# Kernel optimization log

Hardware: AMD Instinct MI355X
Metric: run time of the kernel (lower is better)

The kernel has to match this reference:

```python
import jax, jax.numpy as jnp
import numpy as np

B, R, NB, T = 32, 96, 5, 2048
FEAT_DIM = 64
SPARSITY = 0.2


def _per_band(X, community, W1, b1, W2, b2):
    # X: [R, T] wavelet coeffs for one (batch, band) slice
    n, t = X.shape
    f32 = X.dtype
    # --- functional connectivity (cosine of centered signals == Pearson corr) ---
    Xc = X - X.mean(axis=1, keepdims=True)
    norm = jnp.linalg.norm(Xc, axis=1, keepdims=True)
    norm = jnp.where(norm == 0, 1.0, norm)
    C = (Xc @ Xc.T) / (norm * norm.T)
    C = jnp.nan_to_num(C, nan=0.0)
    C = C * (1.0 - jnp.eye(n, dtype=f32))  # zero diagonal
    # --- quantile sparsification over strict lower triangle ---
    ti, tj = np.tril_indices(n, -1)
    thr = jnp.quantile(jnp.abs(C[ti, tj]), 1.0 - SPARSITY)
    A = C * (jnp.abs(C) >= thr).astype(f32)  # graph_type == 'weighted'
    # --- node features (5-dim, averaged over regions) ---
    mean_f = X.mean(axis=1)
    std_f = jnp.std(X, axis=1, ddof=1)  # torch.std is unbiased
    energy_f = (X ** 2).sum(axis=1)
    maxamp_f = jnp.abs(X).max(axis=1)
    ps = jnp.abs(jnp.fft.fft(X, axis=1)) ** 2
    ps = ps[:, : t // 2]
    s = ps.sum(axis=1, keepdims=True)
    s = jnp.where(s == 0, 1.0, s)
    p = ps / s
    ent_f = -(p * jnp.log(p + 1e-10)).sum(axis=1)
    node5 = jnp.stack([mean_f, std_f, energy_f, maxamp_f, ent_f], axis=1).mean(axis=0)
    # --- graph properties (6-dim) on binarized adjacency ---
    Bm = (A != 0).astype(f32)
    ne = Bm.sum() / 2.0
    density = ne / (n * (n - 1) / 2.0)
    deg = Bm.sum(axis=1)
    avg_deg = deg.mean()
    A2 = Bm @ Bm
    tri = (A2 * Bm).sum() / 6.0
    poss = (deg * (deg - 1.0)).sum() / 2.0
    clus = jnp.where(poss > 0, tri / jnp.where(poss > 0, poss, 1.0), 0.0)
    # global efficiency: safe reciprocal (zero where A+I == 0; original would emit inf)
    denom = Bm + jnp.eye(n, dtype=f32)
    eff = jnp.where(denom > 0, 1.0 / jnp.where(denom > 0, denom, 1.0), 0.0).sum() / (n * (n - 1))
    # approximate modularity with fixed 2-community assignment (deterministic)
    m2 = 2.0 * ne
    m2_safe = jnp.where(m2 > 0, m2, 1.0)
    same = (community[:, None] == community[None, :]) & (~jnp.eye(n, dtype=bool))
    expected = jnp.outer(deg, deg) / m2_safe
    mod = jnp.where(m2 > 0, (same * (Bm - expected)).sum() / m2_safe, 0.0)
    props = jnp.stack([ne, density, avg_deg, clus, eff, mod])
    feat11 = jnp.concatenate([node5, props])  # [11]
    # --- feature encoder MLP (dropout is identity at inference) ---
    h = jnp.maximum(feat11 @ W1.T + b1, 0.0)
    return A, h @ W2.T + b2


def _forward(wavelet_coeffs, frequency_bands, community, W1, b1, W2, b2):
    b, r, nb, t = wavelet_coeffs.shape
    Xs = wavelet_coeffs.transpose(0, 2, 1, 3).reshape(b * nb, r, t)  # [B*NB, R, T]
    A, F = jax.vmap(_per_band, in_axes=(0, None, None, None, None, None))(
        Xs, community, W1, b1, W2, b2)
    return A.reshape(b, nb, r, r), F.reshape(b, nb, -1)


def setup_inputs() -> dict:
    key = jax.random.key(0)
    k0, k1, k2, k3, k4 = jax.random.split(key, 5)
    wavelet_coeffs = jax.random.normal(k0, (B, R, NB, T), dtype=jnp.float32)
    frequency_bands = jax.random.uniform(k1, (NB, 2), dtype=jnp.float32)
    community = jax.random.randint(k2, (R,), 0, 2)
    W1 = jax.random.normal(k3, (32, 11), dtype=jnp.float32) * 0.3
    b1 = jnp.zeros((32,), jnp.float32)
    W2 = jax.random.normal(k4, (FEAT_DIM, 32), dtype=jnp.float32) * 0.18
    b2 = jnp.zeros((FEAT_DIM,), jnp.float32)
    return {"wavelet_coeffs": wavelet_coeffs, "frequency_bands": frequency_bands,
            "community": community, "W1": W1, "b1": b1, "W2": W2, "b2": b2}


def reference(wavelet_coeffs, frequency_bands, community, W1, b1, W2, b2):
    return _forward(wavelet_coeffs, frequency_bands, community, W1, b1, W2, b2)
```

## Files before the change

### kernel.cpp

```cpp
#include <hip/hip_runtime.h>
#include <hip/hip_bf16.h>
#include <math.h>
#include <float.h>

#ifndef M_PI
#define M_PI 3.14159265358979323846
#endif

#define NBANDS 160
#define RR 96
#define TT 2048
#define NTRIL 4560
#define A_ELEMS ((size_t)NBANDS * RR * RR)
#define NBIN 8192
#define MAXCAND 512
#define BKS 64
#define NST (TT / BKS)
#define GPITCH 76
#define FBLK 256

#define PHI(L) ((L) ^ (((L) >> 5) & 31))

typedef float  f32x4  __attribute__((ext_vector_type(4)));
typedef __bf16 bf16x8 __attribute__((ext_vector_type(8)));
typedef __bf16 bf16x4 __attribute__((ext_vector_type(4)));

__device__ inline void blockReduceSum4(double v0, double v1, double v2, double v3,
                                       double* sred, double out[4]) {
    for (int off = 32; off > 0; off >>= 1) {
        v0 += __shfl_down(v0, off, 64);
        v1 += __shfl_down(v1, off, 64);
        v2 += __shfl_down(v2, off, 64);
        v3 += __shfl_down(v3, off, 64);
    }
    int lane = threadIdx.x & 63, wid = threadIdx.x >> 6;
    int nw = blockDim.x >> 6;
    if (lane == 0) {
        sred[wid * 4 + 0] = v0; sred[wid * 4 + 1] = v1;
        sred[wid * 4 + 2] = v2; sred[wid * 4 + 3] = v3;
    }
    __syncthreads();
    if (threadIdx.x < 4) {
        double r = sred[threadIdx.x];
        for (int w = 1; w < nw; w++) r += sred[w * 4 + threadIdx.x];
        sred[nw * 4 + threadIdx.x] = r;
    }
    __syncthreads();
    out[0] = sred[nw * 4 + 0]; out[1] = sred[nw * 4 + 1];
    out[2] = sred[nw * 4 + 2]; out[3] = sred[nw * 4 + 3];
    __syncthreads();
}

__device__ inline void blockReduceSum2(double v0, double v1,
                                       double* sred, double out[2]) {
    for (int off = 32; off > 0; off >>= 1) {
        v0 += __shfl_down(v0, off, 64);
        v1 += __shfl_down(v1, off, 64);
    }
    int lane = threadIdx.x & 63, wid = threadIdx.x >> 6;
    int nw = blockDim.x >> 6;
    if (lane == 0) { sred[wid * 2 + 0] = v0; sred[wid * 2 + 1] = v1; }
    __syncthreads();
    if (threadIdx.x < 2) {
        double r = sred[threadIdx.x];
        for (int w = 1; w < nw; w++) r += sred[w * 2 + threadIdx.x];
        sred[nw * 2 + threadIdx.x] = r;
    }
    __syncthreads();
    out[0] = sred[nw * 2 + 0]; out[1] = sred[nw * 2 + 1];
    __syncthreads();
}

__device__ inline void blockReduceMax2(double v0, double v1,
                                       double* sred, double out[2]) {
    for (int off = 32; off > 0; off >>= 1) {
        v0 = fmax(v0, __shfl_down(v0, off, 64));
        v1 = fmax(v1, __shfl_down(v1, off, 64));
    }
    int lane = threadIdx.x & 63, wid = threadIdx.x >> 6;
    int nw = blockDim.x >> 6;
    if (lane == 0) { sred[wid * 2 + 0] = v0; sred[wid * 2 + 1] = v1; }
    __syncthreads();
    if (threadIdx.x < 2) {
        double r = sred[threadIdx.x];
        for (int w = 1; w < nw; w++) r = fmax(r, sred[w * 2 + threadIdx.x]);
        sred[nw * 2 + threadIdx.x] = r;
    }
    __syncthreads();
    out[0] = sred[nw * 2 + 0]; out[1] = sred[nw * 2 + 1];
    __syncthreads();
}

__global__ void twiddle_kernel(float* tw) {
    int k = blockIdx.x * blockDim.x + threadIdx.x;
    if (k < 1024) {
        double ang = -2.0 * M_PI * (double)k / 2048.0;
        tw[2 * k]     = (float)cos(ang);
        tw[2 * k + 1] = (float)sin(ang);
    }
}

#define BFLY(r1, r2, WR, WI) do { \
    float _wr = (WR), _wi = (WI); \
    float _tr = _wr * yr[r2] - _wi * yi[r2]; \
    float _ti = _wr * yi[r2] + _wi * yr[r2]; \
    yr[r2] = yr[r1] - _tr; yi[r2] = yi[r1] - _ti; \
    yr[r1] += _tr; yi[r1] += _ti; } while (0)

__global__ __launch_bounds__(256) void rowstat_fft_kernel(
    const float* __restrict__ wc, const float* __restrict__ tw,
    double* __restrict__ rowstats)
{
    __shared__ float re[TT];
    __shared__ float im[TT];
    __shared__ double sred[32];
    __shared__ float bcast[4];

    int t = threadIdx.x;
    int g0 = blockIdx.x * 2;
    int g1 = g0 + 1;

    int band = g0 / RR, r0 = g0 % RR;
    int b = band / 5, nb = band % 5;
    size_t base0 = ((size_t)(b * RR + r0) * 5 + nb) * TT;
    size_t base1 = base0 + (size_t)5 * TT;
    const float2* twv = (const float2*)tw;

    float s0 = 0.f, s1 = 0.f, q0 = 0.f, q1 = 0.f, m0 = 0.f, m1 = 0.f;
#pragma unroll
    for (int c = 0; c < 8; c++) {
        int i = t + c * 256;
        float af = wc[base0 + i];
        float bf = wc[base1 + i];
        int P = PHI(i);
        re[P] = af; im[P] = bf;
        s0 += af; s1 += bf;
        q0 = fmaf(af, af, q0); q1 = fmaf(bf, bf, q1);
        m0 = fmaxf(m0, fabsf(af)); m1 = fmaxf(m1, fabsf(bf));
    }
    __syncthreads();

    double S4[4], M2[2];
    blockReduceSum4((double)s0, (double)s1, (double)q0, (double)q1, sred, S4);
    blockReduceMax2((double)m0, (double)m1, sred, M2);
    double SUM0 = S4[0], SUM1 = S4[1], SQ0 = S4[2], SQ1 = S4[3];
    double MX0 = M2[0], MX1 = M2[1];

    float yr[8], yi[8];

#pragma unroll
    for (int j = 0; j < 8; j++) {
        int p = 8 * t + j;
        int L = (int)(__brev((unsigned)p) >> 21);
        int P = PHI(L);
        yr[j] = re[P]; yi[j] = im[P];
    }

    const float RC = 0.70710678f;
    BFLY(0, 1, 1.0f, 0.0f); BFLY(2, 3, 1.0f, 0.0f);
    BFLY(4, 5, 1.0f, 0.0f); BFLY(6, 7, 1.0f, 0.0f);
    BFLY(0, 2, 1.0f, 0.0f); BFLY(1, 3, 0.0f, -1.0f);
    BFLY(4, 6, 1.0f, 0.0f); BFLY(5, 7, 0.0f, -1.0f);
    BFLY(0, 4, 1.0f, 0.0f); BFLY(1, 5, RC, -RC);
    BFLY(2, 6, 0.0f, -1.0f); BFLY(3, 7, -RC, -RC);

    __syncthreads();
#pragma unroll
    for (int j = 0; j < 8; j++) {
        int P = PHI(8 * t + j);
        re[P] = yr[j]; im[P] = yi[j];
    }
    __syncthreads();
    int oo = t & 7;
    int bb64 = 4 * ((t >> 3) & 7) + (t >> 6);
#pragma unroll
    for (int k = 0; k < 8; k++) {
        int P = PHI(64 * bb64 + 8 * k + oo);
        yr[k] = re[P]; yi[k] = im[P];
    }

    {
        float2 w0 = twv[oo << 7];
        BFLY(0, 1, w0.x, w0.y); BFLY(2, 3, w0.x, w0.y);
        BFLY(4, 5, w0.x, w0.y); BFLY(6, 7, w0.x, w0.y);
        float2 wa = twv[oo << 6];
        float2 wb = twv[(oo + 8) << 6];
        BFLY(0, 2, wa.x, wa.y); BFLY(1, 3, wb.x, wb.y);
        BFLY(4, 6, wa.x, wa.y); BFLY(5, 7, wb.x, wb.y);
        float2 wc0 = twv[oo << 5], wc1 = twv[(oo + 8) << 5];
        float2 wc2 = twv[(oo + 16) << 5], wc3 = twv[(oo + 24) << 5];
        BFLY(0, 4, wc0.x, wc0.y);
        BFLY(1, 5, wc1.x, wc1.y);
        BFLY(2, 6, wc2.x, wc2.y);
        BFLY(3, 7, wc3.x, wc3.y);
    }

    __syncthreads();
#pragma unroll
    for (int k = 0; k < 8; k++) {
        int P = PHI(64 * bb64 + 8 * k + oo);
        re[P] = yr[k]; im[P] = yi[k];
    }
    __syncthreads();
    int O3 = t & 63, Wq = t >> 6;
#pragma unroll
    for (int s = 0; s < 2; s++) {
        int B3 = Wq + 4 * s;
#pragma unroll
        for (int k = 0; k < 4; k++) {
            int P = PHI(256 * B3 + 64 * k + O3);
            yr[4 * s + k] = re[P]; yi[4 * s + k] = im[P];
        }
    }

    {
        float2 w0 = twv[O3 << 4];
        float2 wa = twv[O3 << 3];
        float2 wb = twv[(O3 + 64) << 3];
        BFLY(0, 1, w0.x, w0.y); BFLY(2, 3, w0.x, w0.y);
        BFLY(4, 5, w0.x, w0.y); BFLY(6, 7, w0.x, w0.y);
        BFLY(0, 2, wa.x, wa.y); BFLY(1, 3, wb.x, wb.y);
        BFLY(4, 6, wa.x, wa.y); BFLY(5, 7, wb.x, wb.y);
    }

    __syncthreads();
#pragma unroll
    for (int s = 0; s < 2; s++) {
        int B3 = Wq + 4 * s;
#pragma unroll
        for (int k = 0; k < 4; k++) {
            int P = PHI(256 * B3 + 64 * k + O3);
            re[P] = yr[4 * s + k]; im[P] = yi[4 * s + k];
        }
    }
    __syncthreads();
#pragma unroll
    for (int k = 0; k < 8; k++) {
        int P = PHI(256 * k + t);
        yr[k] = re[P]; yi[k] = im[P];
    }

    {
        float2 w0 = twv[t << 2];
        float2 wa = twv[t << 1];
        float2 wb = twv[(t + 256) << 1];
        BFLY(0, 1, w0.x, w0.y); BFLY(2, 3, w0.x, w0.y);
        BFLY(4, 5, w0.x, w0.y); BFLY(6, 7, w0.x, w0.y);
        BFLY(0, 2, wa.x, wa.y); BFLY(1, 3, wb.x, wb.y);
        BFLY(4, 6, wa.x, wa.y); BFLY(5, 7, wb.x, wb.y);
        float2 wf0 = twv[t], wf1 = twv[t + 256];
        float2 wf2 = twv[t + 512], wf3 = twv[t + 768];
        BFLY(0, 4, wf0.x, wf0.y);
        BFLY(1, 5, wf1.x, wf1.y);
        BFLY(2, 6, wf2.x, wf2.y);
        BFLY(3, 7, wf3.x, wf3.y);
    }

    __syncthreads();
#pragma unroll
    for (int k = 0; k < 8; k++) {
        int P = PHI(256 * k + t);
        re[P] = yr[k]; im[P] = yi[k];
    }
    __syncthreads();

    float psa[8], psb[8];
#pragma unroll
    for (int k = 0; k < 8; k++) {
        int q = (2048 - t - 256 * k) & 2047;
        int P = PHI(q);
        float prr = re[P], pii = im[P];
        float sr = yr[k] + prr, di = yi[k] - pii;
        float si = yi[k] + pii, dr = yr[k] - prr;
        psa[k] = 0.25f * (sr * sr + di * di);
        psb[k] = 0.25f * (si * si + dr * dr);
    }

    float la = 0.f, lb = 0.f;
#pragma unroll
    for (int k = 0; k < 8; k++) { la += psa[k]; lb += psb[k]; }
    double SS[2];
    blockReduceSum2((double)la, (double)lb, sred, SS);
    double SAall = SS[0], SBall = SS[1];
    if (t == 0) {
        bcast[0] = psa[0]; bcast[1] = psa[4];
        bcast[2] = psb[0]; bcast[3] = psb[4];
    }
    __syncthreads();
    double Sa = 0.5 * (SAall + (double)bcast[0] - (double)bcast[1]);
    double Sb = 0.5 * (SBall + (double)bcast[2] - (double)bcast[3]);
    if (Sa == 0.0) Sa = 1.0;
    if (Sb == 0.0) Sb = 1.0;
    float invSa = (float)(1.0 / Sa), invSb = (float)(1.0 / Sb);

    float ea = 0.f, eb = 0.f;
#pragma unroll
    for (int k = 0; k < 8; k++) {
        float pa = psa[k] * invSa;
        float pb = psb[k] * invSb;
        ea += pa * __logf(pa + 1e-10f);
        eb += pb * __logf(pb + 1e-10f);
    }
    double EE[2];
    blockReduceSum2((double)ea, (double)eb, sred, EE);
    double EAall = EE[0], EBall = EE[1];

    if (t == 0) {
        float pa0 = psa[0] * invSa, pa4 = psa[4] * invSa;
        float pb0 = psb[0] * invSb, pb4 = psb[4] * invSb;
        double TA = 0.5 * (EAall + (double)(pa0 * __logf(pa0 + 1e-10f))
                                 - (double)(pa4 * __logf(pa4 + 1e-10f)));
        double TB = 0.5 * (EBall + (double)(pb0 * __logf(pb0 + 1e-10f))
                                 - (double)(pb4 * __logf(pb4 + 1e-10f)));
        double mean0 = SUM0 / (double)TT;
        double mean1 = SUM1 / (double)TT;
        double nsq0 = SQ0 - (double)TT * mean0 * mean0; if (nsq0 < 0) nsq0 = 0;
        double nsq1 = SQ1 - (double)TT * mean1 * mean1; if (nsq1 < 0) nsq1 = 0;
        double* w0 = rowstats + (size_t)g0 * 6;
        double* w1 = rowstats + (size_t)g1 * 6;
        double n0 = sqrt(nsq0), n1 = sqrt(nsq1);
        w0[0] = mean0; w0[1] = (n0 == 0.0 ? 1.0 : n0); w0[2] = sqrt(nsq0 / 2047.0);
        w0[3] = SQ0;   w0[4] = MX0;                    w0[5] = -TA;
        w1[0] = mean1; w1[1] = (n1 == 0.0 ? 1.0 : n1); w1[2] = sqrt(nsq1 / 2047.0);
        w1[3] = SQ1;   w1[4] = MX1;                    w1[5] = -TB;
    }
}

#define CVW(BUF, v, row, c4) do { \
    __bf16 _h0 = (__bf16)v.x, _h1 = (__bf16)v.y, _h2 = (__bf16)v.z, _h3 = (__bf16)v.w; \
    __bf16 _l0 = (__bf16)(v.x - (float)_h0), _l1 = (__bf16)(v.y - (float)_h1); \
    __bf16 _l2 = (__bf16)(v.z - (float)_h2), _l3 = (__bf16)(v.w - (float)_h3); \
    *(bf16x4*)&sh_hi[BUF][row][(c4) * 4] = (bf16x4){_h0, _h1, _h2, _h3}; \
    *(bf16x4*)&sh_lo[BUF][row][(c4) * 4] = (bf16x4){_l0, _l1, _l2, _l3}; } while (0)

#define LDFRAG(dst, arr, BUF, row, ko) do { \
    bf16x4 _f0 = *(const bf16x4*)&arr[BUF][row][ko]; \
    bf16x4 _f1 = *(const bf16x4*)&arr[BUF][row][(ko) + 4]; \
    dst = (bf16x8){_f0[0], _f0[1], _f0[2], _f0[3], _f1[0], _f1[1], _f1[2], _f1[3]}; } while (0)

__global__ __launch_bounds__(FBLK) void fused_gram_finalize_kernel(
    const float* __restrict__ wc, const double* __restrict__ rowstats,
    const int* __restrict__ community,
    const float* __restrict__ W1, const float* __restrict__ b1,
    const float* __restrict__ W2, const float* __restrict__ b2,
    float* __restrict__ A_out, float* __restrict__ F_out)
{
    __shared__ __attribute__((aligned(16))) __bf16 sh_hi[2][RR][GPITCH];
    __shared__ __attribute__((aligned(16))) __bf16 sh_lo[2][RR][GPITCH];
    __shared__ float Cs[RR][RR];
    __shared__ int hist[NBIN];
    __shared__ int chunkv[256];
    __shared__ int pchunk[256];
    __shared__ int gpre_s[64];
    __shared__ float cand[MAXCAND];
    __shared__ int ctrl[8];
    __shared__ float selv[2];
    __shared__ double mean_s[RR], inv_s[RR];
    __shared__ int comm_s[RR];
    __shared__ unsigned long long msk[RR][2];
    __shared__ int deg[RR];
    __shared__ double sred[32];
    __shared__ double feat[11];
    __shared__ double hmlp[32];
    __shared__ double thr_s;

    int band = blockIdx.x, t = threadIdx.x;
    int b = band / 5, nb = band % 5;
    size_t bandbase = ((size_t)b * RR * 5 + nb) * TT;
    const double* rsb = rowstats + (size_t)band * RR * 6;

    if (t < RR) {
        mean_s[t] = rsb[t * 6 + 0];
        inv_s[t]  = 1.0 / rsb[t * 6 + 1];
        comm_s[t] = community[t];
    }
    for (int i = t; i < NBIN; i += FBLK) hist[i] = 0;
    if (t == 0) ctrl[3] = 0;

    int wave = t >> 6, lane = t & 63;
    int m16 = lane & 15, quad = lane >> 4;
    int wr = wave >> 1;
    int wcx = wave & 1;

    int row0 = t >> 4,           c40 = t & 15;
    int row1 = (t + 256) >> 4,   c41 = (t + 256) & 15;
    int row2 = (t + 512) >> 4,   c42 = (t + 512) & 15;
    int row3 = (t + 768) >> 4,   c43 = (t + 768) & 15;
    int row4 = (t + 1024) >> 4,  c44 = (t + 1024) & 15;
    int row5 = (t + 1280) >> 4,  c45 = (t + 1280) & 15;
    const float* p0 = wc + bandbase + (size_t)row0 * (5 * TT) + c40 * 4;
    const float* p1 = wc + bandbase + (size_t)row1 * (5 * TT) + c41 * 4;
    const float* p2 = wc + bandbase + (size_t)row2 * (5 * TT) + c42 * 4;
    const float* p3 = wc + bandbase + (size_t)row3 * (5 * TT) + c43 * 4;
    const float* p4 = wc + bandbase + (size_t)row4 * (5 * TT) + c44 * 4;
    const float* p5 = wc + bandbase + (size_t)row5 * (5 * TT) + c45 * 4;

    f32x4 acc[3][3];
#pragma unroll
    for (int rs = 0; rs < 3; rs++)
#pragma unroll
        for (int cs = 0; cs < 3; cs++) acc[rs][cs] = (f32x4){0.f, 0.f, 0.f, 0.f};

    {
        float4 v0 = *(const float4*)(p0);
        float4 v1 = *(const float4*)(p1);
        float4 v2 = *(const float4*)(p2);
        float4 v3 = *(const float4*)(p3);
        float4 v4 = *(const float4*)(p4);
        float4 v5 = *(const float4*)(p5);
        CVW(0, v0, row0, c40); CVW(0, v1, row1, c41);
        CVW(0, v2, row2, c42); CVW(0, v3, row3, c43);
        CVW(0, v4, row4, c44); CVW(0, v5, row5, c45);
    }
    __syncthreads();

    for (int st = 0; st < NST; st++) {
        int cur = st & 1;
        float4 q0, q1, q2, q3, q4, q5;
        bool more = (st + 1 < NST);
        if (more) {
            int k0 = (st + 1) * BKS;
            q0 = *(const float4*)(p0 + k0);
            q1 = *(const float4*)(p1 + k0);
            q2 = *(const float4*)(p2 + k0);
            q3 = *(const float4*)(p3 + k0);
            q4 = *(const float4*)(p4 + k0);
            q5 = *(const float4*)(p5 + k0);
        }
#pragma unroll
        for (int ks = 0; ks < BKS / 32; ks++) {
            int ko = ks * 32 + quad * 8;
            bf16x8 ah[3], al[3];
#pragma unroll
            for (int rs = 0; rs < 3; rs++) {
                int ar = wr * 48 + rs * 16 + m16;
                LDFRAG(ah[rs], sh_hi, cur, ar, ko);
                LDFRAG(al[rs], sh_lo, cur, ar, ko);
            }
#pragma unroll
            for (int cs = 0; cs < 3; cs++) {
                int br = wcx * 48 + cs * 16 + m16;
                bf16x8 bh, bl;
                LDFRAG(bh, sh_hi, cur, br, ko);
                LDFRAG(bl, sh_lo, cur, br, ko);
#pragma unroll
                for (int rs = 0; rs < 3; rs++) {
                    acc[rs][cs] = __builtin_amdgcn_mfma_f32_16x16x32_bf16(ah[rs], bh, acc[rs][cs], 0, 0, 0);
                    acc[rs][cs] = __builtin_amdgcn_mfma_f32_16x16x32_bf16(ah[rs], bl, acc[rs][cs], 0, 0, 0);
                    acc[rs][cs] = __builtin_amdgcn_mfma_f32_16x16x32_bf16(al[rs], bh, acc[rs][cs], 0, 0, 0);
                }
            }
        }
        if (more) {
            int nxt = cur ^ 1;
            CVW(nxt, q0, row0, c40); CVW(nxt, q1, row1, c41);
            CVW(nxt, q2, row2, c42); CVW(nxt, q3, row3, c43);
            CVW(nxt, q4, row4, c44); CVW(nxt, q5, row5, c45);
        }
        __syncthreads();
    }

#pragma unroll
    for (int rs = 0; rs < 3; rs++) {
#pragma unroll
        for (int cs = 0; cs < 3; cs++) {
#pragma unroll
            for (int r = 0; r < 4; r++) {
                int grow = wr * 48 + rs * 16 + quad * 4 + r;
                int gcol = wcx * 48 + cs * 16 + m16;
                double cd = ((double)acc[rs][cs][r]
                             - (double)TT * mean_s[grow] * mean_s[gcol])
                            * (inv_s[grow] * inv_s[gcol]);
                if (grow == gcol) cd = 0.0;
                float cf = (float)cd;
                Cs[grow][gcol] = cf;
                if (gcol < grow) {
                    float val = fabsf(cf);
                    int bin = (int)(val * (float)NBIN);
                    bin = bin > (NBIN - 1) ? (NBIN - 1) : bin;
                    atomicAdd(&hist[bin], 1);
                }
            }
        }
    }
    __syncthreads();

    {
        int cs = 0;
#pragma unroll
        for (int i = 0; i < NBIN / 256; i++) cs += hist[t * (NBIN / 256) + i];
        chunkv[t] = cs;
    }
    __syncthreads();
    if (t < 64) {
        int s4 = chunkv[4 * t] + chunkv[4 * t + 1] + chunkv[4 * t + 2] + chunkv[4 * t + 3];
        int inc = s4;
        for (int d = 1; d < 64; d <<= 1) {
            int u = __shfl_up(inc, d, 64);
            if (t >= d) inc += u;
        }
        gpre_s[t] = inc - s4;
    }
    __syncthreads();
    {
        int base = gpre_s[t >> 2];
        for (int j = (t & ~3); j < t; j++) base += chunkv[j];
        pchunk[t] = base;
    }
    __syncthreads();
    {
        int lo = pchunk[t], hi2 = lo + chunkv[t];
        if (lo <= 3647 && 3647 < hi2) ctrl[4] = t;
        if (lo <= 3648 && 3648 < hi2) ctrl[5] = t;
    }
    __syncthreads();
    {
        int c0 = ctrl[4], c1 = ctrl[5];
        if (t < 32) {
            int binb = c0 * 32;
            int pre = pchunk[c0];
            for (int j = 0; j < t; j++) pre += hist[binb + j];
            int cnt = hist[binb + t];
            if (pre <= 3647 && 3647 < pre + cnt) { ctrl[0] = binb + t; ctrl[2] = pre; }
        } else if (t < 64) {
            int tt2 = t - 32;
            int binb = c1 * 32;
            int pre = pchunk[c1];
            for (int j = 0; j < tt2; j++) pre += hist[binb + j];
            int cnt = hist[binb + tt2];
            if (pre <= 3648 && 3648 < pre + cnt) ctrl[1] = binb + tt2;
        }
    }
    __syncthreads();

    int B0 = ctrl[0], B1 = ctrl[1];
    for (int idx = t; idx < RR * RR; idx += FBLK) {
        int i = idx / RR, j = idx % RR;
        if (j < i) {
            float val = fabsf(Cs[i][j]);
            int bin = (int)(val * (float)NBIN);
            bin = bin > (NBIN - 1) ? (NBIN - 1) : bin;
            if (bin >= B0 && bin <= B1) {
                int k = atomicAdd(&ctrl[3], 1);
                if (k < MAXCAND) cand[k] = val;
            }
        }
    }
    __syncthreads();

    {
        int n = ctrl[3]; if (n > MAXCAND) n = MAXCAND;
        int r0l = 3647 - ctrl[2];
        int r1l = 3648 - ctrl[2];
        for (int i = t; i < n; i += FBLK) {
            float v = cand[i];
            int rank = 0;
            for (int j = 0; j < n; j++) {
                float u = cand[j];
                rank += (u < v || (u == v && j < i)) ? 1 : 0;
            }
            if (rank == r0l) selv[0] = v;
            if (rank == r1l) selv[1] = v;
        }
    }
    __syncthreads();
    if (t == 0) {
        double v0 = (double)selv[0], v1 = (double)selv[1];
        thr_s = v0 + 0.2 * (v1 - v0);
    }
    __syncthreads();
    double thr = thr_s;

    float* Ab = A_out + (size_t)band * (RR * RR);
    for (int idx = t; idx < RR * RR; idx += FBLK) {
        float cf = Cs[idx / RR][idx % RR];
        bool keep = ((double)fabsf(cf) >= thr);
        Ab[idx] = keep ? cf : 0.f;
    }

    for (int i = wave; i < RR; i += 4) {
        float vlo = Cs[i][lane];
        bool klo = ((double)fabsf(vlo) >= thr) && (vlo != 0.f);
        unsigned long long blo = __ballot(klo);
        float vhi = Cs[i][64 + (lane & 31)];
        bool khi = (lane < 32) && ((double)fabsf(vhi) >= thr) && (vhi != 0.f);
        unsigned long long bhi = __ballot(khi) & 0xffffffffull;
        if (lane == 0) {
            msk[i][0] = blo; msk[i][1] = bhi;
            deg[i] = __popcll(blo) + __popcll(bhi);
        }
    }
    __syncthreads();

    double triord = 0, ein = 0, expin = 0;
    for (int idx = t; idx < RR * RR; idx += FBLK) {
        int i = idx / RR, j = idx % RR;
        unsigned long long mi0 = msk[i][0], mi1 = msk[i][1];
        bool bij = (((j < 64) ? (mi0 >> j) : (mi1 >> (j - 64))) & 1ull) != 0;
        if (bij)
            triord += (double)(__popcll(mi0 & msk[j][0]) +
                               __popcll(mi1 & msk[j][1]));
        if (i != j && comm_s[i] == comm_s[j]) {
            ein += bij ? 1.0 : 0.0;
            expin += (double)deg[i] * (double)deg[j];
        }
    }
    double dv = (t < RR) ? (double)deg[t] : 0.0;
    double R1v[4], R2v[4], R3v[2];
    blockReduceSum4(triord, ein, expin, dv, sred, R1v);
    blockReduceSum4((t < RR) ? dv * (dv - 1.0) : 0.0,
                    (t < RR) ? rsb[t * 6 + 0] : 0.0,
                    (t < RR) ? rsb[t * 6 + 2] : 0.0,
                    (t < RR) ? rsb[t * 6 + 3] : 0.0, sred, R2v);
    blockReduceSum2((t < RR) ? rsb[t * 6 + 4] : 0.0,
                    (t < RR) ? rsb[t * 6 + 5] : 0.0, sred, R3v);
    double TRI = R1v[0], EIN = R1v[1], EXPIN = R1v[2], DEGS = R1v[3];
    double POSS2 = R2v[0], N0 = R2v[1], N1 = R2v[2], N2 = R2v[3];
    double N3 = R3v[0], N4 = R3v[1];

    if (t == 0) {
        double ne = 0.5 * DEGS;
        feat[0] = N0 / (double)RR;
        feat[1] = N1 / (double)RR;
        feat[2] = N2 / (double)RR;
        feat[3] = N3 / (double)RR;
        feat[4] = N4 / (double)RR;
        feat[5] = ne;
        feat[6] = ne / (double)NTRIL;
        feat[7] = DEGS / (double)RR;
        double tri = TRI / 6.0, poss = POSS2 * 0.5;
        feat[8] = (poss > 0.0) ? tri / poss : 0.0;
        feat[9] = ((double)RR + DEGS) / ((double)RR * (double)(RR - 1));
        double m2 = DEGS;
        feat[10] = (m2 > 0.0) ? (EIN - EXPIN / m2) / m2 : 0.0;
    }
    __syncthreads();

    if (t < 32) {
        double a = (double)b1[t];
        for (int k = 0; k < 11; k++) a += (double)W1[t * 11 + k] * feat[k];
        hmlp[t] = (a > 0.0) ? a : 0.0;
    }
    __syncthreads();
    if (t < 64) {
        double a = (double)b2[t];
        for (int j = 0; j < 32; j++) a += (double)W2[t * 32 + j] * hmlp[j];
        F_out[(size_t)band * 64 + t] = (float)a;
    }
}

extern "C" void kernel_launch(void* const* d_in, const int* in_sizes, int n_in,
                              void* d_out, int out_size, void* d_ws, size_t ws_size,
                              hipStream_t stream) {
    const float* wc        = (const float*)d_in[0];
    const int*   community = (const int*)d_in[2];
    const float* W1        = (const float*)d_in[3];
    const float* b1        = (const float*)d_in[4];
    const float* W2        = (const float*)d_in[5];
    const float* b2        = (const float*)d_in[6];

    float* A_out = (float*)d_out;
    float* F_out = A_out + A_ELEMS;

    char* ws = (char*)d_ws;
    float*  tw       = (float*)ws;
    double* rowstats = (double*)(ws + 8192);

    hipLaunchKernelGGL(twiddle_kernel, dim3(4), dim3(256), 0, stream, tw);
    hipLaunchKernelGGL(rowstat_fft_kernel, dim3(NBANDS * RR / 2), dim3(256), 0, stream,
                       wc, tw, rowstats);
    hipLaunchKernelGGL(fused_gram_finalize_kernel, dim3(NBANDS), dim3(FBLK), 0, stream,
                       wc, rowstats, community, W1, b1, W2, b2, A_out, F_out);
}
```

Baseline: 303.9 us.

## Double block to 512 threads with split-K across wave groups in Gram GEMM

Raises the fused per-band block from 256 to 512 threads. The eight waves are split into two K-halves: each group runs the bf16 hi/lo MFMA tiles on its own 32-column slice of every 64-wide stage, and the partial accumulators are reduced through shared memory before the correlation epilogue. Each thread now loads half as many global float4s per stage, and the later phases are guarded or re-strided for the larger block. The aim is more waves in flight per CU to hide load and MFMA latency, at the cost of an extra shared-memory reduction with two barriers and possibly lower occupancy.

```diff
diff --git a/kernel.cpp b/kernel.cpp
--- a/kernel.cpp
+++ b/kernel.cpp
@@ -17,7 +17,7 @@
 #define BKS 64
 #define NST (TT / BKS)
 #define GPITCH 76
-#define FBLK 256
+#define FBLK 512
 
 #define PHI(L) ((L) ^ (((L) >> 5) & 31))
 
@@ -359,7 +359,7 @@
     __shared__ int comm_s[RR];
     __shared__ unsigned long long msk[RR][2];
     __shared__ int deg[RR];
-    __shared__ double sred[32];
+    __shared__ double sred[40];
     __shared__ double feat[11];
     __shared__ double hmlp[32];
     __shared__ double thr_s;
@@ -379,21 +379,17 @@
 
     int wave = t >> 6, lane = t & 63;
     int m16 = lane & 15, quad = lane >> 4;
-    int wr = wave >> 1;
-    int wcx = wave & 1;
+    int kw = wave >> 2;
+    int wq = wave & 3;
+    int wr = wq >> 1;
+    int wcx = wq & 1;
 
     int row0 = t >> 4,           c40 = t & 15;
-    int row1 = (t + 256) >> 4,   c41 = (t + 256) & 15;
-    int row2 = (t + 512) >> 4,   c42 = (t + 512) & 15;
-    int row3 = (t + 768) >> 4,   c43 = (t + 768) & 15;
-    int row4 = (t + 1024) >> 4,  c44 = (t + 1024) & 15;
-    int row5 = (t + 1280) >> 4,  c45 = (t + 1280) & 15;
+    int row1 = (t + 512) >> 4,   c41 = (t + 512) & 15;
+    int row2 = (t + 1024) >> 4,  c42 = (t + 1024) & 15;
     const float* p0 = wc + bandbase + (size_t)row0 * (5 * TT) + c40 * 4;
     const float* p1 = wc + bandbase + (size_t)row1 * (5 * TT) + c41 * 4;
     const float* p2 = wc + bandbase + (size_t)row2 * (5 * TT) + c42 * 4;
-    const float* p3 = wc + bandbase + (size_t)row3 * (5 * TT) + c43 * 4;
-    const float* p4 = wc + bandbase + (size_t)row4 * (5 * TT) + c44 * 4;
-    const float* p5 = wc + bandbase + (size_t)row5 * (5 * TT) + c45 * 4;
 
     f32x4 acc[3][3];
 #pragma unroll
@@ -405,31 +401,22 @@
         float4 v0 = *(const float4*)(p0);
         float4 v1 = *(const float4*)(p1);
         float4 v2 = *(const float4*)(p2);
-        float4 v3 = *(const float4*)(p3);
-        float4 v4 = *(const float4*)(p4);
-        float4 v5 = *(const float4*)(p5);
-        CVW(0, v0, row0, c40); CVW(0, v1, row1, c41);
-        CVW(0, v2, row2, c42); CVW(0, v3, row3, c43);
-        CVW(0, v4, row4, c44); CVW(0, v5, row5, c45);
+        CVW(0, v0, row0, c40); CVW(0, v1, row1, c41); CVW(0, v2, row2, c42);
     }
     __syncthreads();
 
     for (int st = 0; st < NST; st++) {
         int cur = st & 1;
-        float4 q0, q1, q2, q3, q4, q5;
+        float4 q0, q1, q2;
         bool more = (st + 1 < NST);
         if (more) {
             int k0 = (st + 1) * BKS;
             q0 = *(const float4*)(p0 + k0);
             q1 = *(const float4*)(p1 + k0);
             q2 = *(const float4*)(p2 + k0);
-            q3 = *(const float4*)(p3 + k0);
-            q4 = *(const float4*)(p4 + k0);
-            q5 = *(const float4*)(p5 + k0);
-        }
-#pragma unroll
-        for (int ks = 0; ks < BKS / 32; ks++) {
-            int ko = ks * 32 + quad * 8;
+        }
+        {
+            int ko = kw * 32 + quad * 8;
             bf16x8 ah[3], al[3];
 #pragma unroll
             for (int rs = 0; rs < 3; rs++) {
@@ -453,39 +440,66 @@
         }
         if (more) {
             int nxt = cur ^ 1;
-            CVW(nxt, q0, row0, c40); CVW(nxt, q1, row1, c41);
-            CVW(nxt, q2, row2, c42); CVW(nxt, q3, row3, c43);
-            CVW(nxt, q4, row4, c44); CVW(nxt, q5, row5, c45);
+            CVW(nxt, q0, row0, c40); CVW(nxt, q1, row1, c41); CVW(nxt, q2, row2, c42);
         }
         __syncthreads();
     }
 
-#pragma unroll
-    for (int rs = 0; rs < 3; rs++) {
-#pragma unroll
-        for (int cs = 0; cs < 3; cs++) {
-#pragma unroll
-            for (int r = 0; r < 4; r++) {
-                int grow = wr * 48 + rs * 16 + quad * 4 + r;
-                int gcol = wcx * 48 + cs * 16 + m16;
-                double cd = ((double)acc[rs][cs][r]
-                             - (double)TT * mean_s[grow] * mean_s[gcol])
-                            * (inv_s[grow] * inv_s[gcol]);
-                if (grow == gcol) cd = 0.0;
-                float cf = (float)cd;
-                Cs[grow][gcol] = cf;
-                if (gcol < grow) {
-                    float val = fabsf(cf);
-                    int bin = (int)(val * (float)NBIN);
-                    bin = bin > (NBIN - 1) ? (NBIN - 1) : bin;
-                    atomicAdd(&hist[bin], 1);
+    if (kw == 1) {
+#pragma unroll
+        for (int rs = 0; rs < 3; rs++)
+#pragma unroll
+            for (int cs = 0; cs < 3; cs++)
+#pragma unroll
+                for (int r = 0; r < 4; r++) {
+                    int grow = wr * 48 + rs * 16 + quad * 4 + r;
+                    int gcol = wcx * 48 + cs * 16 + m16;
+                    Cs[grow][gcol] = acc[rs][cs][r];
+                }
+    }
+    __syncthreads();
+    if (kw == 0) {
+#pragma unroll
+        for (int rs = 0; rs < 3; rs++)
+#pragma unroll
+            for (int cs = 0; cs < 3; cs++)
+#pragma unroll
+                for (int r = 0; r < 4; r++) {
+                    int grow = wr * 48 + rs * 16 + quad * 4 + r;
+                    int gcol = wcx * 48 + cs * 16 + m16;
+                    acc[rs][cs][r] += Cs[grow][gcol];
+                }
+    }
+    __syncthreads();
+
+    if (kw == 0) {
+#pragma unroll
+        for (int rs = 0; rs < 3; rs++) {
+#pragma unroll
+            for (int cs = 0; cs < 3; cs++) {
+#pragma unroll
+                for (int r = 0; r < 4; r++) {
+                    int grow = wr * 48 + rs * 16 + quad * 4 + r;
+                    int gcol = wcx * 48 + cs * 16 + m16;
+                    double cd = ((double)acc[rs][cs][r]
+                                 - (double)TT * mean_s[grow] * mean_s[gcol])
+                                * (inv_s[grow] * inv_s[gcol]);
+                    if (grow == gcol) cd = 0.0;
+                    float cf = (float)cd;
+                    Cs[grow][gcol] = cf;
+                    if (gcol < grow) {
+                        float val = fabsf(cf);
+                        int bin = (int)(val * (float)NBIN);
+                        bin = bin > (NBIN - 1) ? (NBIN - 1) : bin;
+                        atomicAdd(&hist[bin], 1);
+                    }
                 }
             }
         }
     }
     __syncthreads();
 
-    {
+    if (t < 256) {
         int cs = 0;
 #pragma unroll
         for (int i = 0; i < NBIN / 256; i++) cs += hist[t * (NBIN / 256) + i];
@@ -502,13 +516,13 @@
         gpre_s[t] = inc - s4;
     }
     __syncthreads();
-    {
+    if (t < 256) {
         int base = gpre_s[t >> 2];
         for (int j = (t & ~3); j < t; j++) base += chunkv[j];
         pchunk[t] = base;
     }
     __syncthreads();
-    {
+    if (t < 256) {
         int lo = pchunk[t], hi2 = lo + chunkv[t];
         if (lo <= 3647 && 3647 < hi2) ctrl[4] = t;
         if (lo <= 3648 && 3648 < hi2) ctrl[5] = t;
@@ -578,7 +592,7 @@
         Ab[idx] = keep ? cf : 0.f;
     }
 
-    for (int i = wave; i < RR; i += 4) {
+    for (int i = wave; i < RR; i += 8) {
         float vlo = Cs[i][lane];
         bool klo = ((double)fabsf(vlo) >= thr) && (vlo != 0.f);
         unsigned long long blo = __ballot(klo);
```

New measurement: 286.1 us. -5.8%, faster.
